# Optimization experiments

Hardware: AMD Instinct MI355X
Metric: run time of the kernel (lower is better)

## Reference

```python
import jax, jax.numpy as jnp
import numpy as np

B, S, D = 32, 576, 768
G = 24  # sqrt(S)
TEMP = 0.01


def grid_sample_bilinear_zeros(img, grid):
    # img: (B,C,H,W), grid: (B,Hg,Wg,2) in [-1,1]; torch F.grid_sample,
    # mode='bilinear', padding_mode='zeros', align_corners=False
    Bn, C, H, W = img.shape
    gx, gy = grid[..., 0], grid[..., 1]
    ix = ((gx + 1.0) * W - 1.0) * 0.5
    iy = ((gy + 1.0) * H - 1.0) * 0.5
    x0 = jnp.floor(ix); y0 = jnp.floor(iy)
    x1 = x0 + 1.0;      y1 = y0 + 1.0
    wx1 = ix - x0; wx0 = 1.0 - wx1
    wy1 = iy - y0; wy0 = 1.0 - wy1

    def gather(xi, yi):
        valid = (xi >= 0) & (xi <= W - 1) & (yi >= 0) & (yi <= H - 1)
        xc = jnp.clip(xi, 0, W - 1).astype(jnp.int32)
        yc = jnp.clip(yi, 0, H - 1).astype(jnp.int32)
        vals = jax.vmap(lambda im, y, x: im[:, y, x])(img, yc, xc)  # (B,C,Hg,Wg)
        return vals * valid.astype(img.dtype)[:, None, :, :]

    return (gather(x0, y0) * (wx0 * wy0)[:, None]
            + gather(x1, y0) * (wx1 * wy0)[:, None]
            + gather(x0, y1) * (wx0 * wy1)[:, None]
            + gather(x1, y1) * (wx1 * wy1)[:, None])


def key_finder_net(h, W1, b1, W2, b2, W3, b3):
    # fc1 -> relu -> fc2 -> relu -> fc3 -> tanh
    h = jax.nn.relu(h @ W1 + b1)
    h = jax.nn.relu(h @ W2 + b2)
    return jnp.tanh(h @ W3 + b3)


def setup_inputs() -> dict:
    key = jax.random.key(0)
    ks = jax.random.split(key, 16)
    sd = 1.0 / np.sqrt(D)
    inp = {
        'x': jax.random.normal(ks[0], (B, S, D), dtype=jnp.float32),
        'indices': jax.random.randint(ks[1], (B, S), 0, S),
        'Wq': jax.random.normal(ks[2], (D, D), dtype=jnp.float32) * sd,
        'bq': jnp.zeros((D,), jnp.float32),
        'Wk': jax.random.normal(ks[3], (D, D), dtype=jnp.float32) * sd,
        'bk': jnp.zeros((D,), jnp.float32),
        'Wv': jax.random.normal(ks[4], (D, D), dtype=jnp.float32) * sd,
        'bv': jnp.zeros((D,), jnp.float32),
        'W1': jax.random.normal(ks[5], (2 * D, 60), dtype=jnp.float32) / np.sqrt(2 * D),
        'b1': jnp.zeros((60,), jnp.float32),
        'W2': jax.random.normal(ks[6], (60, 60), dtype=jnp.float32) / np.sqrt(60),
        'b2': jnp.zeros((60,), jnp.float32),
        'W3': jax.random.normal(ks[7], (60, 2), dtype=jnp.float32) / np.sqrt(60),
        'b3': jnp.zeros((2,), jnp.float32),
    }
    return inp


def reference(x, indices, Wq, bq, Wk, bk, Wv, bv, W1, b1, W2, b2, W3, b3):
    q = x @ Wq + bq  # (B,S,D)
    k = x @ Wk + bk
    v = x @ Wv + bv

    sample = key_finder_net(jnp.concatenate([q, k], axis=2), W1, b1, W2, b2, W3, b3)  # (B,S,2)
    # torch: cat((sample_x, sample_y), dim=1).reshape(B,G,G,2)
    flat = jnp.concatenate([sample[:, :, 0], sample[:, :, 1]], axis=1)  # (B,2S)
    grid = flat.reshape(B, G, G, 2)

    k_img = jnp.transpose(k, (0, 2, 1)).reshape(B, D, G, G)
    v_img = jnp.transpose(v, (0, 2, 1)).reshape(B, D, G, G)

    sk = grid_sample_bilinear_zeros(k_img, grid)  # (B,D,G,G)
    sv = grid_sample_bilinear_zeros(v_img, grid)
    sampled_key = jnp.transpose(sk.reshape(B, D, G * G), (0, 2, 1))   # (B,S,D)
    sampled_value = jnp.transpose(sv.reshape(B, D, G * G), (0, 2, 1))

    scores = jnp.sum(q * sampled_key, axis=-1)  # (B,S)
    return jax.nn.sigmoid(TEMP * scores)[..., None] * sampled_value
```

## Files before the change

kernel.cpp:

```cpp
#include <hip/hip_runtime.h>

typedef _Float16 f16;
typedef _Float16 f16x8 __attribute__((ext_vector_type(8)));
typedef _Float16 f16x4 __attribute__((ext_vector_type(4)));
typedef float f32x4 __attribute__((ext_vector_type(4)));
typedef float f32x16 __attribute__((ext_vector_type(16)));

constexpr int NB = 32, NS = 576, ND = 768, NG = 24;
constexpr int M_TOT = NB * NS;
constexpr int N_TOT = 3 * ND;

__global__ __launch_bounds__(256) void cast_w_t_kernel(const float* __restrict__ Wq,
                                                       const float* __restrict__ Wk,
                                                       const float* __restrict__ Wv,
                                                       f16* __restrict__ WT) {
  __shared__ float tile[64][65];
  int bt = blockIdx.x;
  int ntile = bt / 12, ktile = bt % 12;
  const float* src = (ntile < 12) ? Wq : ((ntile < 24) ? Wk : Wv);
  int n0 = (ntile % 12) * 64, k0 = ktile * 64;
  int cc = threadIdx.x & 63, rr = threadIdx.x >> 6;
#pragma unroll
  for (int i = 0; i < 16; i++) {
    int k = rr + i * 4;
    tile[cc][k] = src[(size_t)(k0 + k) * ND + n0 + cc];
  }
  __syncthreads();
#pragma unroll
  for (int i = 0; i < 16; i++) {
    int n = rr + i * 4;
    WT[(size_t)(ntile * 64 + n) * ND + k0 + cc] = (f16)tile[n][cc];
  }
}

__global__ __launch_bounds__(256) void wcT_kernel(const float* __restrict__ Wq,
                                                  const float* __restrict__ Wk,
                                                  const float* __restrict__ bq,
                                                  const float* __restrict__ bk,
                                                  const float* __restrict__ W1,
                                                  const float* __restrict__ b1,
                                                  f16* __restrict__ WcT_hi,
                                                  f16* __restrict__ WcT_lo,
                                                  float* __restrict__ bc) {
  __shared__ float part[4][64];
  int wave = threadIdx.x >> 6, lane = threadIdx.x & 63;
  int c = (lane < 60) ? lane : 59;
  int j0 = wave * 192;
  if (blockIdx.x == 768) {
    float acc = 0.f;
    for (int j = j0; j < j0 + 192; j++)
      acc += bq[j] * W1[j * 60 + c] + bk[j] * W1[(ND + j) * 60 + c];
    part[wave][lane] = acc;
    __syncthreads();
    if (wave == 0 && lane < 60)
      bc[lane] = b1[lane] + part[0][lane] + part[1][lane] + part[2][lane] + part[3][lane];
    return;
  }
  int r = blockIdx.x;
  const float* wq = Wq + (size_t)r * ND;
  const float* wk = Wk + (size_t)r * ND;
  float acc = 0.f;
  for (int j = j0; j < j0 + 192; j++)
    acc += wq[j] * W1[j * 60 + c] + wk[j] * W1[(ND + j) * 60 + c];
  part[wave][lane] = acc;
  __syncthreads();
  if (wave == 0 && lane < 60) {
    float v = part[0][lane] + part[1][lane] + part[2][lane] + part[3][lane];
    f16 hi = (f16)v;
    WcT_hi[(size_t)lane * ND + r] = hi;
    WcT_lo[(size_t)lane * ND + r] = (f16)(v - (float)hi);
  }
}

__global__ __launch_bounds__(256) void z1_fused_kernel(const float* __restrict__ x,
                                                       const f16* __restrict__ WcT_hi,
                                                       const f16* __restrict__ WcT_lo,
                                                       const float* __restrict__ bc,
                                                       const float* __restrict__ W2,
                                                       const float* __restrict__ b2,
                                                       const float* __restrict__ W3,
                                                       const float* __restrict__ b3,
                                                       f16* __restrict__ xb,
                                                       float* __restrict__ coords) {
  __shared__ float red[3][16][64];
  __shared__ float htile[16][60];
  int wave = threadIdx.x >> 6, lane = threadIdx.x & 63;
  int q = lane >> 4, r16 = lane & 15;
  int m0 = blockIdx.x * 16;
  int k0 = wave * 192;
  const float* xr = x + (size_t)(m0 + r16) * ND + k0;
  f16* xbr = xb + (size_t)(m0 + r16) * ND + k0;

  f32x4 acc[4];
#pragma unroll
  for (int nf = 0; nf < 4; nf++) acc[nf] = 0.f;

  for (int kk = 0; kk < 192; kk += 32) {
    int ko = kk + q * 8;
    float4 v0 = *(const float4*)(xr + ko);
    float4 v1 = *(const float4*)(xr + ko + 4);
    f16x8 a_hi, a_lo;
    float xv[8] = {v0.x, v0.y, v0.z, v0.w, v1.x, v1.y, v1.z, v1.w};
#pragma unroll
    for (int j = 0; j < 8; j++) {
      f16 h = (f16)xv[j];
      a_hi[j] = h;
      a_lo[j] = (f16)(xv[j] - (float)h);
    }
    *(f16x8*)(xbr + ko) = a_hi;
    f16x8 b_hi[4], b_lo[4];
#pragma unroll
    for (int nf = 0; nf < 4; nf++) {
      size_t off = (size_t)(nf * 16 + r16) * ND + k0 + ko;
      b_hi[nf] = *(const f16x8*)(WcT_hi + off);
      b_lo[nf] = *(const f16x8*)(WcT_lo + off);
    }
#pragma unroll
    for (int nf = 0; nf < 4; nf++) {
      acc[nf] = __builtin_amdgcn_mfma_f32_16x16x32_f16(a_hi, b_hi[nf], acc[nf], 0, 0, 0);
      acc[nf] = __builtin_amdgcn_mfma_f32_16x16x32_f16(a_lo, b_hi[nf], acc[nf], 0, 0, 0);
      acc[nf] = __builtin_amdgcn_mfma_f32_16x16x32_f16(a_hi, b_lo[nf], acc[nf], 0, 0, 0);
    }
  }

  if (wave > 0) {
#pragma unroll
    for (int nf = 0; nf < 4; nf++)
#pragma unroll
      for (int r = 0; r < 4; r++) red[wave - 1][nf * 4 + r][lane] = acc[nf][r];
  }
  __syncthreads();
  if (wave == 0) {
#pragma unroll
    for (int nf = 0; nf < 4; nf++) {
      int col = nf * 16 + r16;
      if (col < 60) {
        float bcv = bc[col];
#pragma unroll
        for (int r = 0; r < 4; r++) {
          float v = acc[nf][r] + red[0][nf * 4 + r][lane] + red[1][nf * 4 + r][lane]
                  + red[2][nf * 4 + r][lane] + bcv;
          htile[q * 4 + r][col] = fmaxf(v, 0.f);
        }
      }
    }
  }
  __syncthreads();

  int c = (lane < 60) ? lane : 59;
  float b2v = b2[c];
  float w30 = W3[c * 2 + 0], w31 = W3[c * 2 + 1];
#pragma unroll
  for (int rr = 0; rr < 4; rr++) {
    int row = wave * 4 + rr;
    float acc2 = b2v;
    for (int j = 0; j < 60; j++) acc2 = fmaf(htile[row][j], W2[j * 60 + c], acc2);
    float h2 = fmaxf(acc2, 0.f);
    float p0 = (lane < 60) ? h2 * w30 : 0.f;
    float p1 = (lane < 60) ? h2 * w31 : 0.f;
#pragma unroll
    for (int o = 32; o > 0; o >>= 1) { p0 += __shfl_down(p0, o); p1 += __shfl_down(p1, o); }
    if (lane == 0) {
      float s0 = tanhf(p0 + b3[0]);
      float s1 = tanhf(p1 + b3[1]);
      int m = m0 + row;
      int b = m / NS, s = m % NS;
      float* cb = coords + (size_t)b * (2 * NS);
      cb[(s >> 1) * 2 + (s & 1)] = s0;
      cb[(288 + (s >> 1)) * 2 + (s & 1)] = s1;
    }
  }
}

__device__ __forceinline__ void async_copy16(const f16* g, f16* l) {
  __builtin_amdgcn_global_load_lds((const __attribute__((address_space(1))) void*)g,
                                   (__attribute__((address_space(3))) void*)l, 16, 0, 0);
}

__global__ __launch_bounds__(256) void gemm_kernel(const f16* __restrict__ A,
                                                   const f16* __restrict__ Bt,
                                                   const float* __restrict__ bq,
                                                   const float* __restrict__ bk,
                                                   const float* __restrict__ bv,
                                                   f16* __restrict__ C) {
  constexpr int BM = 128, BK = 64;
  __shared__ __align__(16) f16 sA[BM * BK];
  __shared__ __align__(16) f16 sB[BM * BK];

  int orig = blockIdx.x;
  int wg = (orig & 7) * 324 + (orig >> 3);
  int bm = wg / 18, bn = wg % 18;
  int tid = threadIdx.x;
  int wave = tid >> 6, lane = tid & 63;
  int wm = (wave >> 1) * 64, wn = (wave & 1) * 64;
  int m0 = bm * BM, n0 = bn * BM;

  int srow = tid >> 3;
  int gchunk = ((tid & 7) ^ (srow & 7) ^ (((srow >> 3) & 3) << 1)) * 8;

  f32x16 acc[2][2];
#pragma unroll
  for (int i = 0; i < 2; i++)
#pragma unroll
    for (int j = 0; j < 2; j++) acc[i][j] = 0.f;

  int r32 = lane & 31, q2 = lane >> 5;
  int fx = (r32 & 7) ^ (((r32 >> 3) & 3) << 1);

  for (int kk = 0; kk < ND; kk += BK) {
#pragma unroll
    for (int ps = 0; ps < 4; ps++) {
      async_copy16(A + (size_t)(m0 + ps * 32 + srow) * ND + kk + gchunk, sA + ps * 2048 + tid * 8);
      async_copy16(Bt + (size_t)(n0 + ps * 32 + srow) * ND + kk + gchunk, sB + ps * 2048 + tid * 8);
    }
    __syncthreads();

#pragma unroll
    for (int ks = 0; ks < 4; ks++) {
      f16x8 aF[2], bF[2];
#pragma unroll
      for (int mt = 0; mt < 2; mt++) {
        int R = wm + mt * 32 + r32;
        aF[mt] = *(const f16x8*)(sA + R * 64 + (((ks * 2 + q2) ^ fx) * 8));
      }
#pragma unroll
      for (int nt = 0; nt < 2; nt++) {
        int R = wn + nt * 32 + r32;
        bF[nt] = *(const f16x8*)(sB + R * 64 + (((ks * 2 + q2) ^ fx) * 8));
      }
#pragma unroll
      for (int mt = 0; mt < 2; mt++)
#pragma unroll
        for (int nt = 0; nt < 2; nt++)
          acc[mt][nt] = __builtin_amdgcn_mfma_f32_32x32x16_f16(bF[nt], aF[mt], acc[mt][nt], 0, 0, 0);
    }
    __syncthreads();
  }

#pragma unroll
  for (int mt = 0; mt < 2; mt++) {
    int gm = m0 + wm + mt * 32 + r32;
#pragma unroll
    for (int nt = 0; nt < 2; nt++) {
#pragma unroll
      for (int g = 0; g < 4; g++) {
        int gn0 = n0 + wn + nt * 32 + 8 * g + 4 * q2;
        const float* bp = (gn0 < ND) ? (bq + gn0)
                        : ((gn0 < 2 * ND) ? (bk + gn0 - ND) : (bv + gn0 - 2 * ND));
        float4 bias = *(const float4*)bp;
        f16x4 o;
        o[0] = (f16)(acc[mt][nt][4 * g + 0] + bias.x);
        o[1] = (f16)(acc[mt][nt][4 * g + 1] + bias.y);
        o[2] = (f16)(acc[mt][nt][4 * g + 2] + bias.z);
        o[3] = (f16)(acc[mt][nt][4 * g + 3] + bias.w);
        *(f16x4*)(C + (size_t)gm * N_TOT + gn0) = o;
      }
    }
  }
}

__global__ __launch_bounds__(256) void sample_kernel(const f16* __restrict__ qkv,
                                                     const float* __restrict__ coords,
                                                     float* __restrict__ out) {
  int wave = threadIdx.x >> 6, t = threadIdx.x & 63;
  int x8 = blockIdx.x & 7;
  int i = blockIdx.x >> 3;
  int b = x8 * 4 + (i / 144);
  int p = (i % 144) * 4 + wave;

  float gx = coords[(size_t)b * (2 * NS) + p * 2 + 0];
  float gy = coords[(size_t)b * (2 * NS) + p * 2 + 1];
  float ix = ((gx + 1.f) * (float)NG - 1.f) * 0.5f;
  float iy = ((gy + 1.f) * (float)NG - 1.f) * 0.5f;
  float x0f = floorf(ix), y0f = floorf(iy);
  float wx1 = ix - x0f, wx0 = 1.f - wx1;
  float wy1 = iy - y0f, wy0 = 1.f - wy1;
  int x0 = (int)x0f, y0 = (int)y0f, x1 = x0 + 1, y1 = y0 + 1;
  bool vx0 = (x0 >= 0) & (x0 <= NG - 1), vx1 = (x1 >= 0) & (x1 <= NG - 1);
  bool vy0 = (y0 >= 0) & (y0 <= NG - 1), vy1 = (y1 >= 0) & (y1 <= NG - 1);
  int cx0 = min(max(x0, 0), NG - 1), cx1 = min(max(x1, 0), NG - 1);
  int cy0 = min(max(y0, 0), NG - 1), cy1 = min(max(y1, 0), NG - 1);
  float w00 = wx0 * wy0 * ((vx0 && vy0) ? 1.f : 0.f);
  float w10 = wx1 * wy0 * ((vx1 && vy0) ? 1.f : 0.f);
  float w01 = wx0 * wy1 * ((vx0 && vy1) ? 1.f : 0.f);
  float w11 = wx1 * wy1 * ((vx1 && vy1) ? 1.f : 0.f);

  size_t base = (size_t)b * NS;
  const f16* r00 = qkv + (base + cy0 * NG + cx0) * N_TOT;
  const f16* r10 = qkv + (base + cy0 * NG + cx1) * N_TOT;
  const f16* r01 = qkv + (base + cy1 * NG + cx0) * N_TOT;
  const f16* r11 = qkv + (base + cy1 * NG + cx1) * N_TOT;
  const f16* qr  = qkv + (base + p) * N_TOT;

  float partial = 0.f;
  float outv[12];
#pragma unroll
  for (int ch = 0; ch < 3; ch++) {
    int d = ch * 256 + t * 4;
    f16x4 k00 = *(const f16x4*)(r00 + ND + d);
    f16x4 k10 = *(const f16x4*)(r10 + ND + d);
    f16x4 k01 = *(const f16x4*)(r01 + ND + d);
    f16x4 k11 = *(const f16x4*)(r11 + ND + d);
    f16x4 v00 = *(const f16x4*)(r00 + 2 * ND + d);
    f16x4 v10 = *(const f16x4*)(r10 + 2 * ND + d);
    f16x4 v01 = *(const f16x4*)(r01 + 2 * ND + d);
    f16x4 v11 = *(const f16x4*)(r11 + 2 * ND + d);
    f16x4 qv  = *(const f16x4*)(qr + d);
#pragma unroll
    for (int j = 0; j < 4; j++) {
      float sk = w00 * (float)k00[j] + w10 * (float)k10[j]
               + w01 * (float)k01[j] + w11 * (float)k11[j];
      float sv = w00 * (float)v00[j] + w10 * (float)v10[j]
               + w01 * (float)v01[j] + w11 * (float)v11[j];
      partial = fmaf((float)qv[j], sk, partial);
      outv[ch * 4 + j] = sv;
    }
  }
#pragma unroll
  for (int o = 32; o > 0; o >>= 1) partial += __shfl_down(partial, o);
  float score = __shfl(partial, 0);
  float sig = 1.f / (1.f + expf(-0.01f * score));
  float* orow = out + (size_t)(base + p) * ND;
#pragma unroll
  for (int ch = 0; ch < 3; ch++) {
    int d = ch * 256 + t * 4;
    float4 st;
    st.x = sig * outv[ch * 4 + 0]; st.y = sig * outv[ch * 4 + 1];
    st.z = sig * outv[ch * 4 + 2]; st.w = sig * outv[ch * 4 + 3];
    *(float4*)(orow + d) = st;
  }
}

extern "C" void kernel_launch(void* const* d_in, const int* in_sizes, int n_in,
                              void* d_out, int out_size, void* d_ws, size_t ws_size,
                              hipStream_t stream) {
  const float* x  = (const float*)d_in[0];
  const float* Wq = (const float*)d_in[2];
  const float* bq = (const float*)d_in[3];
  const float* Wk = (const float*)d_in[4];
  const float* bk = (const float*)d_in[5];
  const float* Wv = (const float*)d_in[6];
  const float* bv = (const float*)d_in[7];
  const float* W1 = (const float*)d_in[8];
  const float* b1 = (const float*)d_in[9];
  const float* W2 = (const float*)d_in[10];
  const float* b2 = (const float*)d_in[11];
  const float* W3 = (const float*)d_in[12];
  const float* b3 = (const float*)d_in[13];
  float* out = (float*)d_out;

  char* ws = (char*)d_ws;
  f16*   xb     = (f16*)(ws);
  f16*   WT     = (f16*)(ws + 28311552);
  f16*   qkv    = (f16*)(ws + 31850496);
  f16*   WcT_hi = (f16*)(ws + 31850496);
  f16*   WcT_lo = (f16*)(ws + 31948800);
  float* bc     = (float*)(ws + 116969472);
  float* coords = (float*)(ws + 121393408);

  cast_w_t_kernel<<<dim3(432), dim3(256), 0, stream>>>(Wq, Wk, Wv, WT);
  wcT_kernel<<<dim3(769), dim3(256), 0, stream>>>(Wq, Wk, bq, bk, W1, b1, WcT_hi, WcT_lo, bc);
  z1_fused_kernel<<<dim3(M_TOT / 16), dim3(256), 0, stream>>>(x, WcT_hi, WcT_lo, bc,
                                                              W2, b2, W3, b3, xb, coords);
  gemm_kernel<<<dim3((M_TOT / 128) * (N_TOT / 128)), dim3(256), 0, stream>>>(xb, WT, bq, bk, bv, qkv);
  sample_kernel<<<dim3(M_TOT / 4), dim3(256), 0, stream>>>(qkv, coords, out);
  (void)in_sizes; (void)n_in; (void)out_size; (void)ws_size;
}
```

Before: 332.1 us.

## Merge prep kernels and run key-finder MLP concurrently with QKV GEMM

Folds the weight transpose-cast, the combined-weight precompute and a new standalone x-to-fp16 cast into a single prep launch. The key-finder MLP blocks and the QKV GEMM blocks are then merged into one launch, so the small MLP work can overlap with the GEMM instead of serialising ahead of it. This removes two launches and the dependency stall between them. In exchange, x is read in a separate pass for the fp16 cast, and the MLP-block buffers are moved so they no longer alias the qkv output.

```diff
diff --git a/kernel.cpp b/kernel.cpp
--- a/kernel.cpp
+++ b/kernel.cpp
@@ -10,43 +10,62 @@
 constexpr int M_TOT = NB * NS;
 constexpr int N_TOT = 3 * ND;
 
-__global__ __launch_bounds__(256) void cast_w_t_kernel(const float* __restrict__ Wq,
-                                                       const float* __restrict__ Wk,
-                                                       const float* __restrict__ Wv,
-                                                       f16* __restrict__ WT) {
-  __shared__ float tile[64][65];
-  int bt = blockIdx.x;
-  int ntile = bt / 12, ktile = bt % 12;
-  const float* src = (ntile < 12) ? Wq : ((ntile < 24) ? Wk : Wv);
-  int n0 = (ntile % 12) * 64, k0 = ktile * 64;
-  int cc = threadIdx.x & 63, rr = threadIdx.x >> 6;
-#pragma unroll
-  for (int i = 0; i < 16; i++) {
-    int k = rr + i * 4;
-    tile[cc][k] = src[(size_t)(k0 + k) * ND + n0 + cc];
-  }
-  __syncthreads();
-#pragma unroll
-  for (int i = 0; i < 16; i++) {
-    int n = rr + i * 4;
-    WT[(size_t)(ntile * 64 + n) * ND + k0 + cc] = (f16)tile[n][cc];
-  }
-}
-
-__global__ __launch_bounds__(256) void wcT_kernel(const float* __restrict__ Wq,
-                                                  const float* __restrict__ Wk,
-                                                  const float* __restrict__ bq,
-                                                  const float* __restrict__ bk,
-                                                  const float* __restrict__ W1,
-                                                  const float* __restrict__ b1,
-                                                  f16* __restrict__ WcT_hi,
-                                                  f16* __restrict__ WcT_lo,
-                                                  float* __restrict__ bc) {
-  __shared__ float part[4][64];
+__global__ __launch_bounds__(256) void prep_kernel(const float* __restrict__ x,
+                                                   const float* __restrict__ Wq,
+                                                   const float* __restrict__ Wk,
+                                                   const float* __restrict__ Wv,
+                                                   const float* __restrict__ bq,
+                                                   const float* __restrict__ bk,
+                                                   const float* __restrict__ W1,
+                                                   const float* __restrict__ b1,
+                                                   f16* __restrict__ WT,
+                                                   f16* __restrict__ WcT_hi,
+                                                   f16* __restrict__ WcT_lo,
+                                                   float* __restrict__ bc,
+                                                   f16* __restrict__ xb) {
+  __shared__ __align__(16) float smem[64 * 65];
+  if (blockIdx.x >= 1201) {
+    size_t base = (size_t)(blockIdx.x - 1201) * 12288;
+    const float* xs = x + base;
+    f16* xd = xb + base;
+#pragma unroll
+    for (int it = 0; it < 6; ++it) {
+      int e = threadIdx.x * 8 + it * 2048;
+      float4 u0 = *(const float4*)(xs + e);
+      float4 u1 = *(const float4*)(xs + e + 4);
+      f16x8 h;
+      h[0] = (f16)u0.x; h[1] = (f16)u0.y; h[2] = (f16)u0.z; h[3] = (f16)u0.w;
+      h[4] = (f16)u1.x; h[5] = (f16)u1.y; h[6] = (f16)u1.z; h[7] = (f16)u1.w;
+      *(f16x8*)(xd + e) = h;
+    }
+    return;
+  }
+  if (blockIdx.x < 432) {
+    float (*tile)[65] = (float(*)[65])smem;
+    int bt = blockIdx.x;
+    int ntile = bt / 12, ktile = bt % 12;
+    const float* src = (ntile < 12) ? Wq : ((ntile < 24) ? Wk : Wv);
+    int n0 = (ntile % 12) * 64, k0 = ktile * 64;
+    int cc = threadIdx.x & 63, rr = threadIdx.x >> 6;
+#pragma unroll
+    for (int i = 0; i < 16; i++) {
+      int k = rr + i * 4;
+      tile[cc][k] = src[(size_t)(k0 + k) * ND + n0 + cc];
+    }
+    __syncthreads();
+#pragma unroll
+    for (int i = 0; i < 16; i++) {
+      int n = rr + i * 4;
+      WT[(size_t)(ntile * 64 + n) * ND + k0 + cc] = (f16)tile[n][cc];
+    }
+    return;
+  }
+  float (*part)[64] = (float(*)[64])smem;
+  int blk = blockIdx.x - 432;
   int wave = threadIdx.x >> 6, lane = threadIdx.x & 63;
   int c = (lane < 60) ? lane : 59;
   int j0 = wave * 192;
-  if (blockIdx.x == 768) {
+  if (blk == 768) {
     float acc = 0.f;
     for (int j = j0; j < j0 + 192; j++)
       acc += bq[j] * W1[j * 60 + c] + bk[j] * W1[(ND + j) * 60 + c];
@@ -56,7 +75,7 @@
       bc[lane] = b1[lane] + part[0][lane] + part[1][lane] + part[2][lane] + part[3][lane];
     return;
   }
-  int r = blockIdx.x;
+  int r = blk;
   const float* wq = Wq + (size_t)r * ND;
   const float* wk = Wk + (size_t)r * ND;
   float acc = 0.f;
@@ -72,122 +91,122 @@
   }
 }
 
-__global__ __launch_bounds__(256) void z1_fused_kernel(const float* __restrict__ x,
-                                                       const f16* __restrict__ WcT_hi,
-                                                       const f16* __restrict__ WcT_lo,
-                                                       const float* __restrict__ bc,
-                                                       const float* __restrict__ W2,
-                                                       const float* __restrict__ b2,
-                                                       const float* __restrict__ W3,
-                                                       const float* __restrict__ b3,
-                                                       f16* __restrict__ xb,
-                                                       float* __restrict__ coords) {
-  __shared__ float red[3][16][64];
-  __shared__ float htile[16][60];
-  int wave = threadIdx.x >> 6, lane = threadIdx.x & 63;
-  int q = lane >> 4, r16 = lane & 15;
-  int m0 = blockIdx.x * 16;
-  int k0 = wave * 192;
-  const float* xr = x + (size_t)(m0 + r16) * ND + k0;
-  f16* xbr = xb + (size_t)(m0 + r16) * ND + k0;
-
-  f32x4 acc[4];
-#pragma unroll
-  for (int nf = 0; nf < 4; nf++) acc[nf] = 0.f;
-
-  for (int kk = 0; kk < 192; kk += 32) {
-    int ko = kk + q * 8;
-    float4 v0 = *(const float4*)(xr + ko);
-    float4 v1 = *(const float4*)(xr + ko + 4);
-    f16x8 a_hi, a_lo;
-    float xv[8] = {v0.x, v0.y, v0.z, v0.w, v1.x, v1.y, v1.z, v1.w};
-#pragma unroll
-    for (int j = 0; j < 8; j++) {
-      f16 h = (f16)xv[j];
-      a_hi[j] = h;
-      a_lo[j] = (f16)(xv[j] - (float)h);
-    }
-    *(f16x8*)(xbr + ko) = a_hi;
-    f16x8 b_hi[4], b_lo[4];
-#pragma unroll
-    for (int nf = 0; nf < 4; nf++) {
-      size_t off = (size_t)(nf * 16 + r16) * ND + k0 + ko;
-      b_hi[nf] = *(const f16x8*)(WcT_hi + off);
-      b_lo[nf] = *(const f16x8*)(WcT_lo + off);
-    }
-#pragma unroll
-    for (int nf = 0; nf < 4; nf++) {
-      acc[nf] = __builtin_amdgcn_mfma_f32_16x16x32_f16(a_hi, b_hi[nf], acc[nf], 0, 0, 0);
-      acc[nf] = __builtin_amdgcn_mfma_f32_16x16x32_f16(a_lo, b_hi[nf], acc[nf], 0, 0, 0);
-      acc[nf] = __builtin_amdgcn_mfma_f32_16x16x32_f16(a_hi, b_lo[nf], acc[nf], 0, 0, 0);
-    }
-  }
-
-  if (wave > 0) {
-#pragma unroll
-    for (int nf = 0; nf < 4; nf++)
-#pragma unroll
-      for (int r = 0; r < 4; r++) red[wave - 1][nf * 4 + r][lane] = acc[nf][r];
-  }
-  __syncthreads();
-  if (wave == 0) {
-#pragma unroll
-    for (int nf = 0; nf < 4; nf++) {
-      int col = nf * 16 + r16;
-      if (col < 60) {
-        float bcv = bc[col];
-#pragma unroll
-        for (int r = 0; r < 4; r++) {
-          float v = acc[nf][r] + red[0][nf * 4 + r][lane] + red[1][nf * 4 + r][lane]
-                  + red[2][nf * 4 + r][lane] + bcv;
-          htile[q * 4 + r][col] = fmaxf(v, 0.f);
-        }
-      }
-    }
-  }
-  __syncthreads();
-
-  int c = (lane < 60) ? lane : 59;
-  float b2v = b2[c];
-  float w30 = W3[c * 2 + 0], w31 = W3[c * 2 + 1];
-#pragma unroll
-  for (int rr = 0; rr < 4; rr++) {
-    int row = wave * 4 + rr;
-    float acc2 = b2v;
-    for (int j = 0; j < 60; j++) acc2 = fmaf(htile[row][j], W2[j * 60 + c], acc2);
-    float h2 = fmaxf(acc2, 0.f);
-    float p0 = (lane < 60) ? h2 * w30 : 0.f;
-    float p1 = (lane < 60) ? h2 * w31 : 0.f;
-#pragma unroll
-    for (int o = 32; o > 0; o >>= 1) { p0 += __shfl_down(p0, o); p1 += __shfl_down(p1, o); }
-    if (lane == 0) {
-      float s0 = tanhf(p0 + b3[0]);
-      float s1 = tanhf(p1 + b3[1]);
-      int m = m0 + row;
-      int b = m / NS, s = m % NS;
-      float* cb = coords + (size_t)b * (2 * NS);
-      cb[(s >> 1) * 2 + (s & 1)] = s0;
-      cb[(288 + (s >> 1)) * 2 + (s & 1)] = s1;
-    }
-  }
-}
-
 __device__ __forceinline__ void async_copy16(const f16* g, f16* l) {
   __builtin_amdgcn_global_load_lds((const __attribute__((address_space(1))) void*)g,
                                    (__attribute__((address_space(3))) void*)l, 16, 0, 0);
 }
 
-__global__ __launch_bounds__(256) void gemm_kernel(const f16* __restrict__ A,
-                                                   const f16* __restrict__ Bt,
-                                                   const float* __restrict__ bq,
-                                                   const float* __restrict__ bk,
-                                                   const float* __restrict__ bv,
-                                                   f16* __restrict__ C) {
+__global__ __launch_bounds__(256) void z1gemm_kernel(const float* __restrict__ x,
+                                                     const f16* __restrict__ xbA,
+                                                     const f16* __restrict__ Bt,
+                                                     const f16* __restrict__ WcT_hi,
+                                                     const f16* __restrict__ WcT_lo,
+                                                     const float* __restrict__ bc,
+                                                     const float* __restrict__ W2,
+                                                     const float* __restrict__ b2,
+                                                     const float* __restrict__ W3,
+                                                     const float* __restrict__ b3,
+                                                     const float* __restrict__ bq,
+                                                     const float* __restrict__ bk,
+                                                     const float* __restrict__ bv,
+                                                     f16* __restrict__ C,
+                                                     float* __restrict__ coords) {
+  __shared__ __align__(16) char smem[32768];
+  if (blockIdx.x < 1152) {
+    float (*red)[16][64] = (float(*)[16][64])smem;
+    float (*htile)[60]   = (float(*)[60])(smem + 12288);
+    int wave = threadIdx.x >> 6, lane = threadIdx.x & 63;
+    int q = lane >> 4, r16 = lane & 15;
+    int m0 = blockIdx.x * 16;
+    int k0 = wave * 192;
+    const float* xr = x + (size_t)(m0 + r16) * ND + k0;
+
+    f32x4 acc[4];
+#pragma unroll
+    for (int nf = 0; nf < 4; nf++) acc[nf] = 0.f;
+
+    for (int kk = 0; kk < 192; kk += 32) {
+      int ko = kk + q * 8;
+      float4 v0 = *(const float4*)(xr + ko);
+      float4 v1 = *(const float4*)(xr + ko + 4);
+      f16x8 a_hi, a_lo;
+      float xv[8] = {v0.x, v0.y, v0.z, v0.w, v1.x, v1.y, v1.z, v1.w};
+#pragma unroll
+      for (int j = 0; j < 8; j++) {
+        f16 h = (f16)xv[j];
+        a_hi[j] = h;
+        a_lo[j] = (f16)(xv[j] - (float)h);
+      }
+      f16x8 b_hi[4], b_lo[4];
+#pragma unroll
+      for (int nf = 0; nf < 4; nf++) {
+        size_t off = (size_t)(nf * 16 + r16) * ND + k0 + ko;
+        b_hi[nf] = *(const f16x8*)(WcT_hi + off);
+        b_lo[nf] = *(const f16x8*)(WcT_lo + off);
+      }
+#pragma unroll
+      for (int nf = 0; nf < 4; nf++) {
+        acc[nf] = __builtin_amdgcn_mfma_f32_16x16x32_f16(a_hi, b_hi[nf], acc[nf], 0, 0, 0);
+        acc[nf] = __builtin_amdgcn_mfma_f32_16x16x32_f16(a_lo, b_hi[nf], acc[nf], 0, 0, 0);
+        acc[nf] = __builtin_amdgcn_mfma_f32_16x16x32_f16(a_hi, b_lo[nf], acc[nf], 0, 0, 0);
+      }
+    }
+
+    if (wave > 0) {
+#pragma unroll
+      for (int nf = 0; nf < 4; nf++)
+#pragma unroll
+        for (int r = 0; r < 4; r++) red[wave - 1][nf * 4 + r][lane] = acc[nf][r];
+    }
+    __syncthreads();
+    if (wave == 0) {
+#pragma unroll
+      for (int nf = 0; nf < 4; nf++) {
+        int col = nf * 16 + r16;
+        if (col < 60) {
+          float bcv = bc[col];
+#pragma unroll
+          for (int r = 0; r < 4; r++) {
+            float v = acc[nf][r] + red[0][nf * 4 + r][lane] + red[1][nf * 4 + r][lane]
+                    + red[2][nf * 4 + r][lane] + bcv;
+            htile[q * 4 + r][col] = fmaxf(v, 0.f);
+          }
+        }
+      }
+    }
+    __syncthreads();
+
+    int c = (lane < 60) ? lane : 59;
+    float b2v = b2[c];
+    float w30 = W3[c * 2 + 0], w31 = W3[c * 2 + 1];
+#pragma unroll
+    for (int rr = 0; rr < 4; rr++) {
+      int row = wave * 4 + rr;
+      float acc2 = b2v;
+      for (int j = 0; j < 60; j++) acc2 = fmaf(htile[row][j], W2[j * 60 + c], acc2);
+      float h2 = fmaxf(acc2, 0.f);
+      float p0 = (lane < 60) ? h2 * w30 : 0.f;
+      float p1 = (lane < 60) ? h2 * w31 : 0.f;
+#pragma unroll
+      for (int o = 32; o > 0; o >>= 1) { p0 += __shfl_down(p0, o); p1 += __shfl_down(p1, o); }
+      if (lane == 0) {
+        float s0 = tanhf(p0 + b3[0]);
+        float s1 = tanhf(p1 + b3[1]);
+        int m = m0 + row;
+        int b = m / NS, s = m % NS;
+        float* cb = coords + (size_t)b * (2 * NS);
+        cb[(s >> 1) * 2 + (s & 1)] = s0;
+        cb[(288 + (s >> 1)) * 2 + (s & 1)] = s1;
+      }
+    }
+    return;
+  }
+
   constexpr int BM = 128, BK = 64;
-  __shared__ __align__(16) f16 sA[BM * BK];
-  __shared__ __align__(16) f16 sB[BM * BK];
-
-  int orig = blockIdx.x;
+  f16* sA = (f16*)smem;
+  f16* sB = (f16*)(smem + 16384);
+
+  int orig = blockIdx.x - 1152;
   int wg = (orig & 7) * 324 + (orig >> 3);
   int bm = wg / 18, bn = wg % 18;
   int tid = threadIdx.x;
@@ -210,7 +229,7 @@
   for (int kk = 0; kk < ND; kk += BK) {
 #pragma unroll
     for (int ps = 0; ps < 4; ps++) {
-      async_copy16(A + (size_t)(m0 + ps * 32 + srow) * ND + kk + gchunk, sA + ps * 2048 + tid * 8);
+      async_copy16(xbA + (size_t)(m0 + ps * 32 + srow) * ND + kk + gchunk, sA + ps * 2048 + tid * 8);
       async_copy16(Bt + (size_t)(n0 + ps * 32 + srow) * ND + kk + gchunk, sB + ps * 2048 + tid * 8);
     }
     __syncthreads();
@@ -353,16 +372,15 @@
   f16*   xb     = (f16*)(ws);
   f16*   WT     = (f16*)(ws + 28311552);
   f16*   qkv    = (f16*)(ws + 31850496);
-  f16*   WcT_hi = (f16*)(ws + 31850496);
-  f16*   WcT_lo = (f16*)(ws + 31948800);
   float* bc     = (float*)(ws + 116969472);
+  f16*   WcT_hi = (f16*)(ws + 117000192);
+  f16*   WcT_lo = (f16*)(ws + 117098496);
   float* coords = (float*)(ws + 121393408);
 
-  cast_w_t_kernel<<<dim3(432), dim3(256), 0, stream>>>(Wq, Wk, Wv, WT);
-  wcT_kernel<<<dim3(769), dim3(256), 0, stream>>>(Wq, Wk, bq, bk, W1, b1, WcT_hi, WcT_lo, bc);
-  z1_fused_kernel<<<dim3(M_TOT / 16), dim3(256), 0, stream>>>(x, WcT_hi, WcT_lo, bc,
-                                                              W2, b2, W3, b3, xb, coords);
-  gemm_kernel<<<dim3((M_TOT / 128) * (N_TOT / 128)), dim3(256), 0, stream>>>(xb, WT, bq, bk, bv, qkv);
+  prep_kernel<<<dim3(432 + 769 + 1152), dim3(256), 0, stream>>>(x, Wq, Wk, Wv, bq, bk, W1, b1,
+                                                                WT, WcT_hi, WcT_lo, bc, xb);
+  z1gemm_kernel<<<dim3(1152 + (M_TOT / 128) * (N_TOT / 128)), dim3(256), 0, stream>>>(
+      x, xb, WT, WcT_hi, WcT_lo, bc, W2, b2, W3, b3, bq, bk, bv, qkv, coords);
   sample_kernel<<<dim3(M_TOT / 4), dim3(256), 0, stream>>>(qkv, coords, out);
   (void)in_sizes; (void)n_in; (void)out_size; (void)ws_size;
 }
```

Result: slower. 408.4 us (+23.0%).
